# Kernel tuning notes

Hardware: AMD Instinct MI355X
Metric: run time of the kernel (lower is better)

Reference implementation:

```python
import jax, jax.numpy as jnp
import numpy as np

F, H1, H2, K, L = 16, 64, 64, 8, 8          # n_features, hidden sizes, num_bins, num_layers
NBP = 3 * K + 1                              # num_bijector_params per feature
RMIN, RMAX = -10.0, 10.0
MIN_BIN, MIN_SLOPE = 1e-4, 1e-4              # distrax RationalQuadraticSpline defaults


def setup_inputs() -> dict:
    key = jax.random.key(0)
    ks = jax.random.split(key, 11)
    B = 131072
    return {
        "x": jax.random.normal(ks[0], (B, F), jnp.float32),
        "W0": jax.random.normal(ks[1], (L, F, F), jnp.float32) * 0.1,
        "b0": jax.random.normal(ks[2], (L, F), jnp.float32) * 0.01,
        "W1": jax.random.normal(ks[3], (L, F, H1), jnp.float32) * 0.1,
        "b1": jax.random.normal(ks[4], (L, H1), jnp.float32) * 0.01,
        "W2": jax.random.normal(ks[5], (L, H1, H2), jnp.float32) * 0.1,
        "b2": jax.random.normal(ks[6], (L, H2), jnp.float32) * 0.01,
        "Wout": jax.random.normal(ks[7], (L, H2, F * NBP), jnp.float32) * 0.05,
        "bout": jax.random.normal(ks[8], (L, F * NBP), jnp.float32) * 0.01,
        # scalar-affine coupling params; scale kept positive (init is ones in the module)
        "scale": jnp.exp(0.05 * jax.random.normal(ks[9], (L, F), jnp.float32)),
        "shift": jax.random.normal(ks[10], (L, F), jnp.float32) * 0.1,
    }


def _rq_spline_fwd(params, x):
    """distrax.RationalQuadraticSpline forward_and_log_det (elementwise).
    params: (B, F, 3K+1), x: (B, F) -> (y, log_det) each (B, F)."""
    uw, uh, ud = params[..., :K], params[..., K:2 * K], params[..., 2 * K:]
    total = RMAX - RMIN
    w = jax.nn.softmax(uw, axis=-1) * (total - K * MIN_BIN) + MIN_BIN   # bin widths
    h = jax.nn.softmax(uh, axis=-1) * (total - K * MIN_BIN) + MIN_BIN   # bin heights
    offset = float(np.log(np.expm1(1.0 - MIN_SLOPE)))                   # softplus(0+offset)=1
    d = jax.nn.softplus(ud + offset) + MIN_SLOPE                        # knot slopes (B,F,K+1)
    zeros = jnp.zeros(w.shape[:-1] + (1,), w.dtype)
    xpos = RMIN + jnp.concatenate([zeros, jnp.cumsum(w, -1)], -1)       # knot x (B,F,K+1)
    ypos = RMIN + jnp.concatenate([zeros, jnp.cumsum(h, -1)], -1)       # knot y (B,F,K+1)
    # per-element bin search
    idx = jnp.clip(jnp.sum((x[..., None] >= xpos).astype(jnp.int32), -1) - 1, 0, K - 1)
    take = lambda a: jnp.take_along_axis(a, idx[..., None], axis=-1)[..., 0]
    xk, xk1 = take(xpos[..., :-1]), take(xpos[..., 1:])
    yk, yk1 = take(ypos[..., :-1]), take(ypos[..., 1:])
    dk, dk1 = take(d[..., :-1]), take(d[..., 1:])
    bw = xk1 - xk
    bh = yk1 - yk
    s = bh / bw                                                          # bin slope
    z = jnp.clip((x - xk) / bw, 0.0, 1.0)
    z1m = 1.0 - z
    den = s + (dk1 + dk - 2.0 * s) * z * z1m
    y = yk + bh * (s * z * z + dk * z * z1m) / den
    num_ld = dk1 * z * z + 2.0 * s * z * z1m + dk * z1m * z1m
    ld = 2.0 * jnp.log(s) + jnp.log(num_ld) - 2.0 * jnp.log(den)
    outside = (x <= RMIN) | (x >= RMAX)                                  # identity outside range
    return jnp.where(outside, x, y), jnp.where(outside, 0.0, ld)


def reference(x, W0, b0, W1, b1, W2, b2, Wout, bout, scale, shift):
    """log_prob of Transformed(base, Inverse(Chain(layers))) == base.log_prob(Chain.fwd(x)) + fwd logdet."""
    B = x.shape[0]
    feat = jnp.arange(F)
    z = x
    logdet = jnp.zeros((B,), x.dtype)
    # distrax.Chain applies the last-appended layer first -> iterate layers in reverse;
    # within layer i: spline coupling (appended second) then scalar-affine coupling.
    for i in reversed(range(L)):
        mask = ((feat + i) % 2).astype(bool)        # True = pass-through / conditioner input
        mz = jnp.where(mask, z, 0.0)
        hid = jnp.tanh(mz @ W0[i] + b0[i])
        hid = jnp.tanh(hid @ W1[i] + b1[i])
        hid = hid @ W2[i] + b2[i]                   # last MLP layer is linear
        p = (hid @ Wout[i] + bout[i]).reshape(B, F, NBP)
        y, ld = _rq_spline_fwd(p, z)
        z = jnp.where(mask, z, y)
        logdet = logdet + jnp.sum(jnp.where(mask, 0.0, ld), axis=-1)
        # scalar affine coupling with all-False mask: transforms every feature
        z = z * scale[i] + shift[i]
        logdet = logdet + jnp.sum(jnp.log(jnp.abs(scale[i])))
    base_lp = -0.5 * jnp.sum(z * z, axis=-1) - 0.5 * F * float(np.log(2.0 * np.pi))
    return base_lp + logdet
```

## Files before the change

### kernel.cpp

```cpp
#include <hip/hip_runtime.h>
#include <math.h>

typedef _Float16 f16;
typedef _Float16 half8 __attribute__((ext_vector_type(8)));
typedef float f32x16 __attribute__((ext_vector_type(16)));

#define DEV __device__ __forceinline__

#define W1F_OFF 0
#define W2F_OFF 16384
#define WOF_OFF 81920
#define BOF_OFF 344064
#define SUMLOG_OFF 352256

#define H0_OFF    0
#define H0_STRIDE 48
#define H_OFF     12288
#define H_STRIDE  144
#define P_OFF     49152
#define P_STRIDE  116
#define LDS_BYTES 78848

DEV float frcp(float x){ return __builtin_amdgcn_rcpf(x); }
DEV float fexp(float x){ return __expf(x); }
DEV float flog(float x){ return __logf(x); }

DEV float ftanh(float x){
  float cx = fminf(fmaxf(x, -15.f), 15.f);
  float e  = fexp(2.f * cx);
  return (e - 1.f) * frcp(e + 1.f);
}

DEV f32x16 zero16(){ f32x16 r;
#pragma unroll
  for (int i = 0; i < 16; ++i) r[i] = 0.f;
  return r; }

DEV void rq_spline(const float p[25], float xv, float &y_out, float &ld_out)
{
  float ew[8]; float sw = 0.f;
#pragma unroll
  for (int k = 0; k < 8; ++k){ ew[k] = fexp(p[k]); sw += ew[k]; }
  float rw = frcp(sw) * 19.9992f;

  float xpos[9];
  xpos[0] = -10.f;
#pragma unroll
  for (int k = 0; k < 8; ++k) xpos[k + 1] = xpos[k] + fmaf(ew[k], rw, 1e-4f);

  int idx = 0;
#pragma unroll
  for (int j = 1; j < 8; ++j) idx += (xv >= xpos[j]) ? 1 : 0;

  float xk = xpos[0], ewk = ew[0];
#pragma unroll
  for (int j = 1; j < 8; ++j){
    bool sel = (idx >= j);
    xk  = sel ? xpos[j] : xk;
    ewk = sel ? ew[j]   : ewk;
  }
  float bw = fmaf(ewk, rw, 1e-4f);

  float eh[8]; float shs = 0.f;
#pragma unroll
  for (int k = 0; k < 8; ++k){ eh[k] = fexp(p[8 + k]); shs += eh[k]; }
  float rh = frcp(shs) * 19.9992f;

  float S = 0.f, ehk = eh[0];
#pragma unroll
  for (int k = 1; k < 8; ++k){
    bool sel = (idx >= k);
    S   += sel ? eh[k - 1] : 0.f;
    ehk  = sel ? eh[k]     : ehk;
  }
  float yk = fmaf(S, rh, fmaf((float)idx, 1e-4f, -10.f));
  float bh = fmaf(ehk, rh, 1e-4f);

  float uA = p[16], uB = p[17];
#pragma unroll
  for (int j = 1; j < 8; ++j){
    bool sel = (idx >= j);
    uA = sel ? p[16 + j] : uA;
    uB = sel ? p[17 + j] : uB;
  }
  float vA = uA + 0.54116666f;
  float dk  = fmaxf(vA, 0.f) + flog(1.f + fexp(-fabsf(vA))) + 1e-4f;
  float vB = uB + 0.54116666f;
  float dk1 = fmaxf(vB, 0.f) + flog(1.f + fexp(-fabsf(vB))) + 1e-4f;

  float rbw = frcp(bw);
  float s   = bh * rbw;
  float zf  = fminf(fmaxf((xv - xk) * rbw, 0.f), 1.f);
  float z1  = 1.f - zf;
  float zz  = zf * zf, z01 = zf * z1;
  float den = s + (dk1 + dk - 2.f * s) * z01;
  float rden = frcp(den);
  float yv  = yk + bh * (s * zz + dk * z01) * rden;
  float num = dk1 * zz + 2.f * s * z01 + dk * z1 * z1;
  float ldv = flog(s * s * num * rden * rden);

  bool outside = (xv <= -10.f) || (xv >= 10.f);
  y_out  = outside ? xv : yv;
  ld_out = outside ? 0.f : ldv;
}

extern "C" __global__ void __launch_bounds__(256)
prep_kernel(const float* __restrict__ W1, const float* __restrict__ W2,
            const float* __restrict__ Wo, const float* __restrict__ bout,
            const float* __restrict__ scale, char* __restrict__ ws)
{
  int tid = blockIdx.x * 256 + threadIdx.x;
  if (tid < 1024){
    int fi = tid >> 6, lane = tid & 63;
    int l = fi >> 1, nt = fi & 1;
    int n = nt * 32 + (lane & 31), khi = lane >> 5;
    half8 h;
#pragma unroll
    for (int j = 0; j < 8; ++j){ int k = khi * 8 + j; h[j] = (f16)W1[l * 1024 + k * 64 + n]; }
    *(half8*)(ws + W1F_OFF + fi * 1024 + lane * 16) = h;
  } else if (tid < 5120){
    int idx = tid - 1024;
    int fi = idx >> 6, lane = idx & 63;
    int l = fi >> 3, kt = (fi >> 1) & 3, nt = fi & 1;
    int n = nt * 32 + (lane & 31), khi = lane >> 5;
    half8 h;
#pragma unroll
    for (int j = 0; j < 8; ++j){ int k = kt * 16 + khi * 8 + j; h[j] = (f16)W2[l * 4096 + k * 64 + n]; }
    *(half8*)(ws + W2F_OFF + fi * 1024 + lane * 16) = h;
  } else if (tid < 21504){
    int idx = tid - 5120;
    int fi = idx >> 6, lane = idx & 63;
    int l = fi >> 5, u = (fi >> 2) & 7, kt = fi & 3;
    int f = (l & 1) + 2 * u;
    int c = lane & 31, khi = lane >> 5;
    half8 h;
#pragma unroll
    for (int j = 0; j < 8; ++j){
      int k = kt * 16 + khi * 8 + j;
      float v = (c < 25) ? Wo[l * 25600 + k * 400 + f * 25 + c] : 0.f;
      h[j] = (f16)v;
    }
    *(half8*)(ws + WOF_OFF + fi * 1024 + lane * 16) = h;
  } else if (tid < 23552){
    int idx = tid - 21504;
    int l = idx >> 8, u = (idx >> 5) & 7, c = idx & 31;
    int f = (l & 1) + 2 * u;
    float v = (c < 25) ? bout[l * 400 + f * 25 + c] : 0.f;
    ((float*)(ws + BOF_OFF))[idx] = v;
  } else if (tid == 23552){
    float acc = 0.f;
    for (int i = 0; i < 128; ++i) acc += logf(fabsf(scale[i]));
    *(float*)(ws + SUMLOG_OFF) = acc;
  }
}

template<int PAR>
DEV void layer_mfma(int l,
                    const float* __restrict__ W0, const float* __restrict__ b0,
                    const float* __restrict__ b1v, const float* __restrict__ b2v,
                    const float* __restrict__ scv, const float* __restrict__ shv,
                    const char* __restrict__ ws, char* lds,
                    float (&z)[16], float &logdet,
                    int t, int lane, int wv, int ln31, int khi)
{
  const float* w0  = W0 + l * 256;
  const float* bb0 = b0 + l * 16;
  const int rowbase = khi * 4;

  const half8* W1F = (const half8*)(ws + W1F_OFF);
  const half8* W2F = (const half8*)(ws + W2F_OFF);
  half8 w1f[2];
#pragma unroll
  for (int nt = 0; nt < 2; ++nt) w1f[nt] = W1F[(l * 2 + nt) * 64 + lane];
  half8 w2f[8];
#pragma unroll
  for (int kt = 0; kt < 4; ++kt)
#pragma unroll
    for (int nt = 0; nt < 2; ++nt)
      w2f[kt * 2 + nt] = W2F[((l * 4 + kt) * 2 + nt) * 64 + lane];
  float bias1[2], bias2[2];
#pragma unroll
  for (int nt = 0; nt < 2; ++nt){
    bias1[nt] = b1v[l * 64 + nt * 32 + ln31];
    bias2[nt] = b2v[l * 64 + nt * 32 + ln31];
  }

  float h0[16];
#pragma unroll
  for (int j = 0; j < 16; ++j) h0[j] = bb0[j];
#pragma unroll
  for (int u = 0; u < 8; ++u){
    const int f = (1 - PAR) + 2 * u;
    const float v = z[f];
#pragma unroll
    for (int j = 0; j < 16; ++j) h0[j] = fmaf(v, w0[f * 16 + j], h0[j]);
  }
  {
    half8 lo, hi;
#pragma unroll
    for (int j = 0; j < 8; ++j){ lo[j] = (f16)ftanh(h0[j]); hi[j] = (f16)ftanh(h0[8 + j]); }
    *(half8*)(lds + H0_OFF + t * H0_STRIDE)      = lo;
    *(half8*)(lds + H0_OFF + t * H0_STRIDE + 16) = hi;
  }

  half8 a0[2];
#pragma unroll
  for (int mt = 0; mt < 2; ++mt){
    int s = wv * 64 + mt * 32 + ln31;
    a0[mt] = *(const half8*)(lds + H0_OFF + s * H0_STRIDE + khi * 16);
  }
  f32x16 d1[2][2];
#pragma unroll
  for (int mt = 0; mt < 2; ++mt)
#pragma unroll
    for (int nt = 0; nt < 2; ++nt) d1[mt][nt] = zero16();
#pragma unroll
  for (int nt = 0; nt < 2; ++nt)
#pragma unroll
    for (int mt = 0; mt < 2; ++mt)
      d1[mt][nt] = __builtin_amdgcn_mfma_f32_32x32x16_f16(a0[mt], w1f[nt], d1[mt][nt], 0, 0, 0);
#pragma unroll
  for (int mt = 0; mt < 2; ++mt)
#pragma unroll
    for (int nt = 0; nt < 2; ++nt)
#pragma unroll
      for (int i = 0; i < 16; ++i){
        int row = (i & 3) + 8 * (i >> 2) + rowbase;
        int s = wv * 64 + mt * 32 + row;
        float v = ftanh(d1[mt][nt][i] + bias1[nt]);
        *(f16*)(lds + H_OFF + s * H_STRIDE + (nt * 32 + ln31) * 2) = (f16)v;
      }

  half8 a1[2][4];
#pragma unroll
  for (int mt = 0; mt < 2; ++mt){
    int s = wv * 64 + mt * 32 + ln31;
#pragma unroll
    for (int kt = 0; kt < 4; ++kt)
      a1[mt][kt] = *(const half8*)(lds + H_OFF + s * H_STRIDE + kt * 32 + khi * 16);
  }
  f32x16 d2[2][2];
#pragma unroll
  for (int mt = 0; mt < 2; ++mt)
#pragma unroll
    for (int nt = 0; nt < 2; ++nt) d2[mt][nt] = zero16();
#pragma unroll
  for (int kt = 0; kt < 4; ++kt)
#pragma unroll
    for (int nt = 0; nt < 2; ++nt)
#pragma unroll
      for (int mt = 0; mt < 2; ++mt)
        d2[mt][nt] = __builtin_amdgcn_mfma_f32_32x32x16_f16(a1[mt][kt], w2f[kt * 2 + nt], d2[mt][nt], 0, 0, 0);

  const half8* WOF = (const half8*)(ws + WOF_OFF);
  const float* BOF = (const float*)(ws + BOF_OFF);
  half8 bfn[4];
#pragma unroll
  for (int kt = 0; kt < 4; ++kt) bfn[kt] = WOF[((l * 8 + 0) * 4 + kt) * 64 + lane];
  float biasn = BOF[(l * 8 + 0) * 32 + ln31];

#pragma unroll
  for (int mt = 0; mt < 2; ++mt)
#pragma unroll
    for (int nt = 0; nt < 2; ++nt)
#pragma unroll
      for (int i = 0; i < 16; ++i){
        int row = (i & 3) + 8 * (i >> 2) + rowbase;
        int s = wv * 64 + mt * 32 + row;
        float v = d2[mt][nt][i] + bias2[nt];
        *(f16*)(lds + H_OFF + s * H_STRIDE + (nt * 32 + ln31) * 2) = (f16)v;
      }

  half8 a2[2][4];
#pragma unroll
  for (int mt = 0; mt < 2; ++mt){
    int s = wv * 64 + mt * 32 + ln31;
#pragma unroll
    for (int kt = 0; kt < 4; ++kt)
      a2[mt][kt] = *(const half8*)(lds + H_OFF + s * H_STRIDE + kt * 32 + khi * 16);
  }

#pragma unroll 1
  for (int u = 0; u < 8; ++u){
    half8 bfc[4];
#pragma unroll
    for (int kt = 0; kt < 4; ++kt) bfc[kt] = bfn[kt];
    float biasp = biasn;
    if (u < 7){
#pragma unroll
      for (int kt = 0; kt < 4; ++kt) bfn[kt] = WOF[((l * 8 + u + 1) * 4 + kt) * 64 + lane];
      biasn = BOF[(l * 8 + u + 1) * 32 + ln31];
    }

    const int f = PAR + 2 * u;
    f32x16 dp[2];
    dp[0] = zero16(); dp[1] = zero16();
#pragma unroll
    for (int kt = 0; kt < 4; ++kt)
#pragma unroll
      for (int mt = 0; mt < 2; ++mt)
        dp[mt] = __builtin_amdgcn_mfma_f32_32x32x16_f16(a2[mt][kt], bfc[kt], dp[mt], 0, 0, 0);

    if (ln31 < 25){
#pragma unroll
      for (int mt = 0; mt < 2; ++mt)
#pragma unroll
        for (int i = 0; i < 16; ++i){
          int row = (i & 3) + 8 * (i >> 2) + rowbase;
          int s = wv * 64 + mt * 32 + row;
          *(float*)(lds + P_OFF + s * P_STRIDE + ln31 * 4) = dp[mt][i] + biasp;
        }
    }
    float p[25];
#pragma unroll
    for (int j = 0; j < 25; ++j)
      p[j] = *(const float*)(lds + P_OFF + t * P_STRIDE + j * 4);
    float y, ld;
    rq_spline(p, z[f], y, ld);
    z[f] = y;
    logdet += ld;
  }

  const float* scp = scv + l * 16;
  const float* shp = shv + l * 16;
#pragma unroll
  for (int j = 0; j < 16; ++j)
    z[j] = fmaf(z[j], scp[j], shp[j]);
}

extern "C" __global__ void __launch_bounds__(256, 2)
flow_kernel(const float* __restrict__ x,
            const float* __restrict__ W0, const float* __restrict__ b0,
            const float* __restrict__ b1v, const float* __restrict__ b2v,
            const float* __restrict__ scv, const float* __restrict__ shv,
            const char* __restrict__ ws, float* __restrict__ out, int B)
{
  extern __shared__ char lds[];
  const int t    = threadIdx.x;
  const int lane = t & 63;
  const int wv   = t >> 6;
  const int ln31 = lane & 31;
  const int khi  = lane >> 5;
  const int g    = blockIdx.x * 256 + t;

  float z[16];
  const float4* xv = reinterpret_cast<const float4*>(x + (size_t)g * 16);
  float4 a0 = xv[0], a1 = xv[1], a2 = xv[2], a3 = xv[3];
  z[0]=a0.x; z[1]=a0.y; z[2]=a0.z; z[3]=a0.w;
  z[4]=a1.x; z[5]=a1.y; z[6]=a1.z; z[7]=a1.w;
  z[8]=a2.x; z[9]=a2.y; z[10]=a2.z; z[11]=a2.w;
  z[12]=a3.x; z[13]=a3.y; z[14]=a3.z; z[15]=a3.w;

  float logdet = 0.f;
  for (int l = 7; l >= 0; --l){
    if (l & 1) layer_mfma<1>(l, W0, b0, b1v, b2v, scv, shv, ws, lds, z, logdet, t, lane, wv, ln31, khi);
    else       layer_mfma<0>(l, W0, b0, b1v, b2v, scv, shv, ws, lds, z, logdet, t, lane, wv, ln31, khi);
  }

  float sumlog = *(const float*)(ws + SUMLOG_OFF);
  float ss = 0.f;
#pragma unroll
  for (int j = 0; j < 16; ++j) ss = fmaf(z[j], z[j], ss);
  out[g] = -0.5f * ss - 14.7030165f + logdet + sumlog;
}

extern "C" void kernel_launch(void* const* d_in, const int* in_sizes, int n_in,
                              void* d_out, int out_size, void* d_ws, size_t ws_size,
                              hipStream_t stream)
{
  const float* x    = (const float*)d_in[0];
  const float* W0   = (const float*)d_in[1];
  const float* b0   = (const float*)d_in[2];
  const float* W1   = (const float*)d_in[3];
  const float* b1   = (const float*)d_in[4];
  const float* W2   = (const float*)d_in[5];
  const float* b2   = (const float*)d_in[6];
  const float* Wout = (const float*)d_in[7];
  const float* bout = (const float*)d_in[8];
  const float* scale= (const float*)d_in[9];
  const float* shift= (const float*)d_in[10];

  int B = in_sizes[0] / 16;

  hipLaunchKernelGGL(prep_kernel, dim3(93), dim3(256), 0, stream,
                     W1, W2, Wout, bout, scale, (char*)d_ws);

  hipLaunchKernelGGL(flow_kernel, dim3(B / 256), dim3(256), LDS_BYTES, stream,
                     x, W0, b0, b1, b2, scale, shift,
                     (const char*)d_ws, (float*)d_out, B);
}
```

Before: 212.6 us.

## Software-pipeline output MFMA with spline eval, fold biases into accumulators

The output-projection loop is restructured so the MFMA for feature u+1 is issued and written to LDS after the current parameters are loaded into registers, letting matrix work overlap the scalar spline math for feature u. Biases now initialise the MFMA accumulators instead of being added after the multiply, and tanh is rewritten as 1-2/(e^{2x}+1) without clamping. The aim is to hide MFMA latency behind ALU-heavy spline evaluation and save a few instructions. Reading P into registers before overwriting relies on per-thread ordering within the wave, so LDS reuse correctness depends on each wave touching only its own rows.

```diff
diff --git a/kernel.cpp b/kernel.cpp
--- a/kernel.cpp
+++ b/kernel.cpp
@@ -26,15 +26,10 @@
 DEV float flog(float x){ return __logf(x); }
 
 DEV float ftanh(float x){
-  float cx = fminf(fmaxf(x, -15.f), 15.f);
-  float e  = fexp(2.f * cx);
-  return (e - 1.f) * frcp(e + 1.f);
-}
-
-DEV f32x16 zero16(){ f32x16 r;
-#pragma unroll
-  for (int i = 0; i < 16; ++i) r[i] = 0.f;
-  return r; }
+  float e = fexp(2.f * x);
+  float r = frcp(e + 1.f);
+  return fmaf(-2.f, r, 1.f);
+}
 
 DEV void rq_spline(const float p[25], float xv, float &y_out, float &ld_out)
 {
@@ -213,7 +208,9 @@
 #pragma unroll
   for (int mt = 0; mt < 2; ++mt)
 #pragma unroll
-    for (int nt = 0; nt < 2; ++nt) d1[mt][nt] = zero16();
+    for (int nt = 0; nt < 2; ++nt)
+#pragma unroll
+      for (int i = 0; i < 16; ++i) d1[mt][nt][i] = bias1[nt];
 #pragma unroll
   for (int nt = 0; nt < 2; ++nt)
 #pragma unroll
@@ -227,7 +224,7 @@
       for (int i = 0; i < 16; ++i){
         int row = (i & 3) + 8 * (i >> 2) + rowbase;
         int s = wv * 64 + mt * 32 + row;
-        float v = ftanh(d1[mt][nt][i] + bias1[nt]);
+        float v = ftanh(d1[mt][nt][i]);
         *(f16*)(lds + H_OFF + s * H_STRIDE + (nt * 32 + ln31) * 2) = (f16)v;
       }
 
@@ -243,7 +240,9 @@
 #pragma unroll
   for (int mt = 0; mt < 2; ++mt)
 #pragma unroll
-    for (int nt = 0; nt < 2; ++nt) d2[mt][nt] = zero16();
+    for (int nt = 0; nt < 2; ++nt)
+#pragma unroll
+      for (int i = 0; i < 16; ++i) d2[mt][nt][i] = bias2[nt];
 #pragma unroll
   for (int kt = 0; kt < 4; ++kt)
 #pragma unroll
@@ -267,7 +266,7 @@
       for (int i = 0; i < 16; ++i){
         int row = (i & 3) + 8 * (i >> 2) + rowbase;
         int s = wv * 64 + mt * 32 + row;
-        float v = d2[mt][nt][i] + bias2[nt];
+        float v = d2[mt][nt][i];
         *(f16*)(lds + H_OFF + s * H_STRIDE + (nt * 32 + ln31) * 2) = (f16)v;
       }
 
@@ -280,27 +279,17 @@
       a2[mt][kt] = *(const half8*)(lds + H_OFF + s * H_STRIDE + kt * 32 + khi * 16);
   }
 
-#pragma unroll 1
-  for (int u = 0; u < 8; ++u){
-    half8 bfc[4];
-#pragma unroll
-    for (int kt = 0; kt < 4; ++kt) bfc[kt] = bfn[kt];
-    float biasp = biasn;
-    if (u < 7){
-#pragma unroll
-      for (int kt = 0; kt < 4; ++kt) bfn[kt] = WOF[((l * 8 + u + 1) * 4 + kt) * 64 + lane];
-      biasn = BOF[(l * 8 + u + 1) * 32 + ln31];
-    }
-
-    const int f = PAR + 2 * u;
+  {
     f32x16 dp[2];
-    dp[0] = zero16(); dp[1] = zero16();
+#pragma unroll
+    for (int mt = 0; mt < 2; ++mt)
+#pragma unroll
+      for (int i = 0; i < 16; ++i) dp[mt][i] = biasn;
 #pragma unroll
     for (int kt = 0; kt < 4; ++kt)
 #pragma unroll
       for (int mt = 0; mt < 2; ++mt)
-        dp[mt] = __builtin_amdgcn_mfma_f32_32x32x16_f16(a2[mt][kt], bfc[kt], dp[mt], 0, 0, 0);
-
+        dp[mt] = __builtin_amdgcn_mfma_f32_32x32x16_f16(a2[mt][kt], bfn[kt], dp[mt], 0, 0, 0);
     if (ln31 < 25){
 #pragma unroll
       for (int mt = 0; mt < 2; ++mt)
@@ -308,13 +297,50 @@
         for (int i = 0; i < 16; ++i){
           int row = (i & 3) + 8 * (i >> 2) + rowbase;
           int s = wv * 64 + mt * 32 + row;
-          *(float*)(lds + P_OFF + s * P_STRIDE + ln31 * 4) = dp[mt][i] + biasp;
+          *(float*)(lds + P_OFF + s * P_STRIDE + ln31 * 4) = dp[mt][i];
         }
     }
+  }
+#pragma unroll
+  for (int kt = 0; kt < 4; ++kt) bfn[kt] = WOF[((l * 8 + 1) * 4 + kt) * 64 + lane];
+  biasn = BOF[(l * 8 + 1) * 32 + ln31];
+
+#pragma unroll 1
+  for (int u = 0; u < 8; ++u){
     float p[25];
 #pragma unroll
     for (int j = 0; j < 25; ++j)
       p[j] = *(const float*)(lds + P_OFF + t * P_STRIDE + j * 4);
+
+    if (u < 7){
+      f32x16 dp[2];
+#pragma unroll
+      for (int mt = 0; mt < 2; ++mt)
+#pragma unroll
+        for (int i = 0; i < 16; ++i) dp[mt][i] = biasn;
+#pragma unroll
+      for (int kt = 0; kt < 4; ++kt)
+#pragma unroll
+        for (int mt = 0; mt < 2; ++mt)
+          dp[mt] = __builtin_amdgcn_mfma_f32_32x32x16_f16(a2[mt][kt], bfn[kt], dp[mt], 0, 0, 0);
+      if (ln31 < 25){
+#pragma unroll
+        for (int mt = 0; mt < 2; ++mt)
+#pragma unroll
+          for (int i = 0; i < 16; ++i){
+            int row = (i & 3) + 8 * (i >> 2) + rowbase;
+            int s = wv * 64 + mt * 32 + row;
+            *(float*)(lds + P_OFF + s * P_STRIDE + ln31 * 4) = dp[mt][i];
+          }
+      }
+      if (u < 6){
+#pragma unroll
+        for (int kt = 0; kt < 4; ++kt) bfn[kt] = WOF[((l * 8 + u + 2) * 4 + kt) * 64 + lane];
+        biasn = BOF[(l * 8 + u + 2) * 32 + ln31];
+      }
+    }
+
+    const int f = PAR + 2 * u;
     float y, ld;
     rq_spline(p, z[f], y, ld);
     z[f] = y;
```

Result: no change. 211.0 us (-0.7%).

## Map each sample to a lane pair, halving per-wave tiles and LDS footprint

Applied to the files above, without the earlier changes.

Each wave now handles 32 samples instead of 64. The two half-waves (khi) split the spline work: lane pairs process the low and high feature groups, each evaluating 4 of the 8 features per layer, and the results are exchanged with a cross-half shuffle. The first MLP layer's A operand is built directly in registers, which removes an LDS round-trip. Biases are folded into the MFMA accumulator init, and tanh is simplified to one exp and one rcp. LDS use shrinks to a per-wave 6.4KB chunk and launch bounds rise to 4 blocks per SU to increase occupancy, at the cost of twice as many blocks and duplicated MLP MFMA work per sample.

```diff
diff --git a/kernel.cpp b/kernel.cpp
--- a/kernel.cpp
+++ b/kernel.cpp
@@ -13,28 +13,21 @@
 #define BOF_OFF 344064
 #define SUMLOG_OFF 352256
 
-#define H0_OFF    0
-#define H0_STRIDE 48
-#define H_OFF     12288
+#define WCHUNK    6400
 #define H_STRIDE  144
-#define P_OFF     49152
-#define P_STRIDE  116
-#define LDS_BYTES 78848
+#define P_SLOT    3200
+#define P_STRIDE  100
+#define LDS_BYTES 25600
 
 DEV float frcp(float x){ return __builtin_amdgcn_rcpf(x); }
 DEV float fexp(float x){ return __expf(x); }
 DEV float flog(float x){ return __logf(x); }
 
 DEV float ftanh(float x){
-  float cx = fminf(fmaxf(x, -15.f), 15.f);
-  float e  = fexp(2.f * cx);
-  return (e - 1.f) * frcp(e + 1.f);
-}
-
-DEV f32x16 zero16(){ f32x16 r;
-#pragma unroll
-  for (int i = 0; i < 16; ++i) r[i] = 0.f;
-  return r; }
+  float e = fexp(2.f * x);
+  float r = frcp(e + 1.f);
+  return fmaf(-2.f, r, 1.f);
+}
 
 DEV void rq_spline(const float p[25], float xv, float &y_out, float &ld_out)
 {
@@ -159,9 +152,9 @@
                     const float* __restrict__ W0, const float* __restrict__ b0,
                     const float* __restrict__ b1v, const float* __restrict__ b2v,
                     const float* __restrict__ scv, const float* __restrict__ shv,
-                    const char* __restrict__ ws, char* lds,
+                    const char* __restrict__ ws, char* wlds ,
                     float (&z)[16], float &logdet,
-                    int t, int lane, int wv, int ln31, int khi)
+                    int lane, int ln31, int khi)
 {
   const float* w0  = W0 + l * 256;
   const float* bb0 = b0 + l * 16;
@@ -172,12 +165,6 @@
   half8 w1f[2];
 #pragma unroll
   for (int nt = 0; nt < 2; ++nt) w1f[nt] = W1F[(l * 2 + nt) * 64 + lane];
-  half8 w2f[8];
-#pragma unroll
-  for (int kt = 0; kt < 4; ++kt)
-#pragma unroll
-    for (int nt = 0; nt < 2; ++nt)
-      w2f[kt * 2 + nt] = W2F[((l * 4 + kt) * 2 + nt) * 64 + lane];
   float bias1[2], bias2[2];
 #pragma unroll
   for (int nt = 0; nt < 2; ++nt){
@@ -195,130 +182,113 @@
 #pragma unroll
     for (int j = 0; j < 16; ++j) h0[j] = fmaf(v, w0[f * 16 + j], h0[j]);
   }
-  {
-    half8 lo, hi;
-#pragma unroll
-    for (int j = 0; j < 8; ++j){ lo[j] = (f16)ftanh(h0[j]); hi[j] = (f16)ftanh(h0[8 + j]); }
-    *(half8*)(lds + H0_OFF + t * H0_STRIDE)      = lo;
-    *(half8*)(lds + H0_OFF + t * H0_STRIDE + 16) = hi;
-  }
-
-  half8 a0[2];
-#pragma unroll
-  for (int mt = 0; mt < 2; ++mt){
-    int s = wv * 64 + mt * 32 + ln31;
-    a0[mt] = *(const half8*)(lds + H0_OFF + s * H0_STRIDE + khi * 16);
-  }
-  f32x16 d1[2][2];
-#pragma unroll
-  for (int mt = 0; mt < 2; ++mt)
-#pragma unroll
-    for (int nt = 0; nt < 2; ++nt) d1[mt][nt] = zero16();
-#pragma unroll
-  for (int nt = 0; nt < 2; ++nt)
-#pragma unroll
-    for (int mt = 0; mt < 2; ++mt)
-      d1[mt][nt] = __builtin_amdgcn_mfma_f32_32x32x16_f16(a0[mt], w1f[nt], d1[mt][nt], 0, 0, 0);
-#pragma unroll
-  for (int mt = 0; mt < 2; ++mt)
+  half8 a0;
+#pragma unroll
+  for (int j = 0; j < 8; ++j){
+    float hv = khi ? h0[j + 8] : h0[j];
+    a0[j] = (f16)ftanh(hv);
+  }
+
+  f32x16 d1[2];
+#pragma unroll
+  for (int nt = 0; nt < 2; ++nt)
+#pragma unroll
+    for (int i = 0; i < 16; ++i) d1[nt][i] = bias1[nt];
+#pragma unroll
+  for (int nt = 0; nt < 2; ++nt)
+    d1[nt] = __builtin_amdgcn_mfma_f32_32x32x16_f16(a0, w1f[nt], d1[nt], 0, 0, 0);
+
+  half8 w2f[8];
+#pragma unroll
+  for (int kt = 0; kt < 4; ++kt)
 #pragma unroll
     for (int nt = 0; nt < 2; ++nt)
+      w2f[kt * 2 + nt] = W2F[((l * 4 + kt) * 2 + nt) * 64 + lane];
+
+#pragma unroll
+  for (int nt = 0; nt < 2; ++nt)
+#pragma unroll
+    for (int i = 0; i < 16; ++i){
+      int row = (i & 3) + 8 * (i >> 2) + rowbase;
+      *(f16*)(wlds + row * H_STRIDE + (nt * 32 + ln31) * 2) = (f16)ftanh(d1[nt][i]);
+    }
+
+  half8 a1[4];
+#pragma unroll
+  for (int kt = 0; kt < 4; ++kt)
+    a1[kt] = *(const half8*)(wlds + ln31 * H_STRIDE + kt * 32 + khi * 16);
+  f32x16 d2[2];
+#pragma unroll
+  for (int nt = 0; nt < 2; ++nt)
+#pragma unroll
+    for (int i = 0; i < 16; ++i) d2[nt][i] = bias2[nt];
+#pragma unroll
+  for (int kt = 0; kt < 4; ++kt)
+#pragma unroll
+    for (int nt = 0; nt < 2; ++nt)
+      d2[nt] = __builtin_amdgcn_mfma_f32_32x32x16_f16(a1[kt], w2f[kt * 2 + nt], d2[nt], 0, 0, 0);
+#pragma unroll
+  for (int nt = 0; nt < 2; ++nt)
+#pragma unroll
+    for (int i = 0; i < 16; ++i){
+      int row = (i & 3) + 8 * (i >> 2) + rowbase;
+      *(f16*)(wlds + row * H_STRIDE + (nt * 32 + ln31) * 2) = (f16)d2[nt][i];
+    }
+
+  half8 a2[4];
+#pragma unroll
+  for (int kt = 0; kt < 4; ++kt)
+    a2[kt] = *(const half8*)(wlds + ln31 * H_STRIDE + kt * 32 + khi * 16);
+
+  const half8* WOF = (const half8*)(ws + WOF_OFF);
+  const float* BOF = (const float*)(ws + BOF_OFF);
+#pragma unroll 1
+  for (int it = 0; it < 4; ++it){
+    half8 bfA[4], bfB[4];
+#pragma unroll
+    for (int kt = 0; kt < 4; ++kt){
+      bfA[kt] = WOF[((l * 8 + it) * 4 + kt) * 64 + lane];
+      bfB[kt] = WOF[((l * 8 + it + 4) * 4 + kt) * 64 + lane];
+    }
+    float biasA = BOF[(l * 8 + it) * 32 + ln31];
+    float biasB = BOF[(l * 8 + it + 4) * 32 + ln31];
+
+    f32x16 dpA, dpB;
+#pragma unroll
+    for (int i = 0; i < 16; ++i){ dpA[i] = biasA; dpB[i] = biasB; }
+#pragma unroll
+    for (int kt = 0; kt < 4; ++kt){
+      dpA = __builtin_amdgcn_mfma_f32_32x32x16_f16(a2[kt], bfA[kt], dpA, 0, 0, 0);
+      dpB = __builtin_amdgcn_mfma_f32_32x32x16_f16(a2[kt], bfB[kt], dpB, 0, 0, 0);
+    }
+    if (ln31 < 25){
 #pragma unroll
       for (int i = 0; i < 16; ++i){
         int row = (i & 3) + 8 * (i >> 2) + rowbase;
-        int s = wv * 64 + mt * 32 + row;
-        float v = ftanh(d1[mt][nt][i] + bias1[nt]);
-        *(f16*)(lds + H_OFF + s * H_STRIDE + (nt * 32 + ln31) * 2) = (f16)v;
+        *(float*)(wlds + row * P_STRIDE + ln31 * 4)          = dpA[i];
+        *(float*)(wlds + P_SLOT + row * P_STRIDE + ln31 * 4) = dpB[i];
       }
-
-  half8 a1[2][4];
-#pragma unroll
-  for (int mt = 0; mt < 2; ++mt){
-    int s = wv * 64 + mt * 32 + ln31;
-#pragma unroll
-    for (int kt = 0; kt < 4; ++kt)
-      a1[mt][kt] = *(const half8*)(lds + H_OFF + s * H_STRIDE + kt * 32 + khi * 16);
-  }
-  f32x16 d2[2][2];
-#pragma unroll
-  for (int mt = 0; mt < 2; ++mt)
-#pragma unroll
-    for (int nt = 0; nt < 2; ++nt) d2[mt][nt] = zero16();
-#pragma unroll
-  for (int kt = 0; kt < 4; ++kt)
-#pragma unroll
-    for (int nt = 0; nt < 2; ++nt)
-#pragma unroll
-      for (int mt = 0; mt < 2; ++mt)
-        d2[mt][nt] = __builtin_amdgcn_mfma_f32_32x32x16_f16(a1[mt][kt], w2f[kt * 2 + nt], d2[mt][nt], 0, 0, 0);
-
-  const half8* WOF = (const half8*)(ws + WOF_OFF);
-  const float* BOF = (const float*)(ws + BOF_OFF);
-  half8 bfn[4];
-#pragma unroll
-  for (int kt = 0; kt < 4; ++kt) bfn[kt] = WOF[((l * 8 + 0) * 4 + kt) * 64 + lane];
-  float biasn = BOF[(l * 8 + 0) * 32 + ln31];
-
-#pragma unroll
-  for (int mt = 0; mt < 2; ++mt)
-#pragma unroll
-    for (int nt = 0; nt < 2; ++nt)
-#pragma unroll
-      for (int i = 0; i < 16; ++i){
-        int row = (i & 3) + 8 * (i >> 2) + rowbase;
-        int s = wv * 64 + mt * 32 + row;
-        float v = d2[mt][nt][i] + bias2[nt];
-        *(f16*)(lds + H_OFF + s * H_STRIDE + (nt * 32 + ln31) * 2) = (f16)v;
-      }
-
-  half8 a2[2][4];
-#pragma unroll
-  for (int mt = 0; mt < 2; ++mt){
-    int s = wv * 64 + mt * 32 + ln31;
-#pragma unroll
-    for (int kt = 0; kt < 4; ++kt)
-      a2[mt][kt] = *(const half8*)(lds + H_OFF + s * H_STRIDE + kt * 32 + khi * 16);
-  }
-
-#pragma unroll 1
-  for (int u = 0; u < 8; ++u){
-    half8 bfc[4];
-#pragma unroll
-    for (int kt = 0; kt < 4; ++kt) bfc[kt] = bfn[kt];
-    float biasp = biasn;
-    if (u < 7){
-#pragma unroll
-      for (int kt = 0; kt < 4; ++kt) bfn[kt] = WOF[((l * 8 + u + 1) * 4 + kt) * 64 + lane];
-      biasn = BOF[(l * 8 + u + 1) * 32 + ln31];
-    }
-
-    const int f = PAR + 2 * u;
-    f32x16 dp[2];
-    dp[0] = zero16(); dp[1] = zero16();
-#pragma unroll
-    for (int kt = 0; kt < 4; ++kt)
-#pragma unroll
-      for (int mt = 0; mt < 2; ++mt)
-        dp[mt] = __builtin_amdgcn_mfma_f32_32x32x16_f16(a2[mt][kt], bfc[kt], dp[mt], 0, 0, 0);
-
-    if (ln31 < 25){
-#pragma unroll
-      for (int mt = 0; mt < 2; ++mt)
-#pragma unroll
-        for (int i = 0; i < 16; ++i){
-          int row = (i & 3) + 8 * (i >> 2) + rowbase;
-          int s = wv * 64 + mt * 32 + row;
-          *(float*)(lds + P_OFF + s * P_STRIDE + ln31 * 4) = dp[mt][i] + biasp;
-        }
-    }
+    }
+    const char* pb = wlds + khi * P_SLOT + ln31 * P_STRIDE;
     float p[25];
 #pragma unroll
-    for (int j = 0; j < 25; ++j)
-      p[j] = *(const float*)(lds + P_OFF + t * P_STRIDE + j * 4);
+    for (int j = 0; j < 25; ++j) p[j] = *(const float*)(pb + j * 4);
+
+    float xlo = z[PAR + 2 * it], xhi = z[PAR + 2 * it + 8];
+    float xin = khi ? xhi : xlo;
     float y, ld;
-    rq_spline(p, z[f], y, ld);
-    z[f] = y;
+    rq_spline(p, xin, y, ld);
     logdet += ld;
+    z[PAR + 2 * it]     = khi ? xlo : y;
+    z[PAR + 2 * it + 8] = khi ? y : xhi;
+  }
+
+#pragma unroll
+  for (int it = 0; it < 4; ++it){
+    float mine  = khi ? z[PAR + 2 * it + 8] : z[PAR + 2 * it];
+    float other = __shfl_xor(mine, 32, 64);
+    z[PAR + 2 * it]     = khi ? other : z[PAR + 2 * it];
+    z[PAR + 2 * it + 8] = khi ? z[PAR + 2 * it + 8] : other;
   }
 
   const float* scp = scv + l * 16;
@@ -328,7 +298,7 @@
     z[j] = fmaf(z[j], scp[j], shp[j]);
 }
 
-extern "C" __global__ void __launch_bounds__(256, 2)
+extern "C" __global__ void __launch_bounds__(256, 4)
 flow_kernel(const float* __restrict__ x,
             const float* __restrict__ W0, const float* __restrict__ b0,
             const float* __restrict__ b1v, const float* __restrict__ b2v,
@@ -341,7 +311,10 @@
   const int wv   = t >> 6;
   const int ln31 = lane & 31;
   const int khi  = lane >> 5;
-  const int g    = blockIdx.x * 256 + t;
+  char* wlds = lds + wv * WCHUNK;
+
+  const int sid = wv * 32 + ln31;
+  const int g   = blockIdx.x * 128 + sid;
 
   float z[16];
   const float4* xv = reinterpret_cast<const float4*>(x + (size_t)g * 16);
@@ -353,15 +326,18 @@
 
   float logdet = 0.f;
   for (int l = 7; l >= 0; --l){
-    if (l & 1) layer_mfma<1>(l, W0, b0, b1v, b2v, scv, shv, ws, lds, z, logdet, t, lane, wv, ln31, khi);
-    else       layer_mfma<0>(l, W0, b0, b1v, b2v, scv, shv, ws, lds, z, logdet, t, lane, wv, ln31, khi);
-  }
+    if (l & 1) layer_mfma<1>(l, W0, b0, b1v, b2v, scv, shv, ws, wlds, z, logdet, lane, ln31, khi);
+    else       layer_mfma<0>(l, W0, b0, b1v, b2v, scv, shv, ws, wlds, z, logdet, lane, ln31, khi);
+  }
+
+  float ldtot = logdet + __shfl_xor(logdet, 32, 64);
 
   float sumlog = *(const float*)(ws + SUMLOG_OFF);
   float ss = 0.f;
 #pragma unroll
   for (int j = 0; j < 16; ++j) ss = fmaf(z[j], z[j], ss);
-  out[g] = -0.5f * ss - 14.7030165f + logdet + sumlog;
+  if (khi == 0)
+    out[g] = -0.5f * ss - 14.7030165f + ldtot + sumlog;
 }
 
 extern "C" void kernel_launch(void* const* d_in, const int* in_sizes, int n_in,
@@ -385,7 +361,7 @@
   hipLaunchKernelGGL(prep_kernel, dim3(93), dim3(256), 0, stream,
                      W1, W2, Wout, bout, scale, (char*)d_ws);
 
-  hipLaunchKernelGGL(flow_kernel, dim3(B / 256), dim3(256), LDS_BYTES, stream,
+  hipLaunchKernelGGL(flow_kernel, dim3(B / 128), dim3(256), LDS_BYTES, stream,
                      x, W0, b0, b1, b2, scale, shift,
                      (const char*)d_ws, (float*)d_out, B);
 }
```

Result: no change. 216.4 us (+1.8%).
